# Performance work log

Measured on AMD Instinct MI355X. Metric: run time of the kernel, lower is better.

The kernel has to match this reference:

```python
import jax, jax.numpy as jnp
import numpy as np

B, T, NE = 8, 256, 64
H = 512
NH = 4
NTOKS = 32000
VOCAB = 32000


def setup_inputs() -> dict:
    key = jax.random.key(0)
    ks = jax.random.split(key, 20)
    s = 0.02
    return {
        "outp": jax.random.randint(ks[0], (B, T), 0, NTOKS),
        "ents": jax.random.normal(ks[1], (B, NE, H), jnp.float32),
        "entlens": jax.random.randint(ks[2], (B,), 1, NE),
        "emb": jax.random.normal(ks[3], (NTOKS, H), jnp.float32) * s,
        "W_ih": jax.random.normal(ks[4], (4 * H, 2 * H), jnp.float32) * s,
        "W_hh": jax.random.normal(ks[5], (4 * H, H), jnp.float32) * s,
        "b_ih": jnp.zeros((4 * H,), jnp.float32),
        "b_hh": jnp.zeros((4 * H,), jnp.float32),
        "Wq": jax.random.normal(ks[6], (H, H), jnp.float32) * s,
        "Wk": jax.random.normal(ks[7], (H, H), jnp.float32) * s,
        "Wv": jax.random.normal(ks[8], (H, H), jnp.float32) * s,
        "out_W": jax.random.normal(ks[9], (VOCAB, 2 * H), jnp.float32) * s,
        "out_b": jnp.zeros((VOCAB,), jnp.float32),
        "sw_W": jax.random.normal(ks[10], (1, 2 * H), jnp.float32) * s,
        "sw_b": jnp.zeros((1,), jnp.float32),
        "mattn_W": jax.random.normal(ks[11], (H, 2 * H), jnp.float32) * s,
        "mattn_b": jnp.zeros((H,), jnp.float32),
    }


def reference(outp, ents, entlens, emb, W_ih, W_hh, b_ih, b_hh, Wq, Wk, Wv,
              out_W, out_b, sw_W, sw_b, mattn_W, mattn_b):
    b, ne, h = ents.shape
    hd = h // NH
    # maskFromList: valid where arange(ne) <= entlens; True = masked out
    invalid = jnp.arange(ne)[None, :] > entlens[:, None]  # [B, NE]
    neg = jnp.float32(-1e30)

    hx0 = ents.mean(axis=1)  # glob init (non-graph path)
    cx0 = hx0
    # precompute K, V per head (keys = ents)
    K = (ents @ Wk.T).reshape(b, ne, NH, hd)
    V = (ents @ Wv.T).reshape(b, ne, NH, hd)
    scale = 1.0 / jnp.sqrt(jnp.float32(h))  # GraphWriter scales by sqrt(full key_dim)

    def mha(hx):
        q = (hx @ Wq.T).reshape(b, NH, hd)
        att = jnp.einsum('bhd,bnhd->bhn', q, K) * scale
        att = jnp.where(invalid[:, None, :], neg, att)
        att = jax.nn.softmax(att, axis=-1)
        return jnp.einsum('bhn,bnhd->bhd', att, V).reshape(b, h)

    e_t = jnp.swapaxes(emb[outp], 0, 1)  # [T, B, H]

    def step(carry, k):
        hx, cx, a = carry
        prev = jnp.concatenate([a, k], axis=1)  # [B, 2H]
        gates = prev @ W_ih.T + b_ih + hx @ W_hh.T + b_hh
        i, f, g, o = jnp.split(gates, 4, axis=1)
        cx = jax.nn.sigmoid(f) * cx + jax.nn.sigmoid(i) * jnp.tanh(g)
        hx = jax.nn.sigmoid(o) * jnp.tanh(cx)
        a = mha(hx)
        return (hx, cx, a), jnp.concatenate([hx, a], axis=1)

    _, outs = jax.lax.scan(step, (hx0, cx0, jnp.zeros_like(hx0)), e_t)
    l = jnp.swapaxes(outs, 0, 1)  # [B, T, 2H]

    s = jax.nn.sigmoid(l @ sw_W.T + sw_b)                     # [B, T, 1]
    o = jax.nn.softmax(l @ out_W.T + out_b, axis=2) * s       # [B, T, V]
    # MatrixAttn pointer distribution over entities
    dec = l @ mattn_W.T + mattn_b                             # [B, T, H]
    unnorm = jnp.einsum('bth,bnh->btn', dec, ents)
    unnorm = jnp.where(invalid[:, None, :], neg, unnorm)
    z = jax.nn.softmax(unnorm, axis=2) * (1.0 - s)            # [B, T, NE]
    full = jnp.concatenate([o, z], axis=2) + 1e-6
    return jnp.log(full), z
```

## Files before the change

### kernel.cpp

```cpp
#include <hip/hip_runtime.h>
#include <cstdint>

#define TT 256
#define BB 8
#define NE 64
#define HH 512
#define VOCAB 32000
#define G4 2048
#define RS 32064
#define MROWS 2048
#define SCALE 0.044194173824159216f

typedef _Float16 h2 __attribute__((ext_vector_type(2)));
typedef _Float16 h8 __attribute__((ext_vector_type(8)));
typedef float f4 __attribute__((ext_vector_type(4)));
typedef unsigned long long u64;

__device__ inline float sigf(float x){ return 1.f/(1.f+__expf(-x)); }

__device__ inline u64 g64load(const u64* p){
  return __hip_atomic_load((u64*)p, __ATOMIC_RELAXED, __HIP_MEMORY_SCOPE_AGENT);
}
__device__ inline void g64store(u64* p, u64 v){
  __hip_atomic_store(p, v, __ATOMIC_RELAXED, __HIP_MEMORY_SCOPE_AGENT);
}

__global__ __launch_bounds__(256) void cast_k(const float* __restrict__ src, _Float16* __restrict__ dst,
    int total, int src_ld, int src_off, int dst_ld, int dst_off, int cshift, int lo, float mul, int tr)
{
  int i = blockIdx.x*256 + threadIdx.x;
  if (i >= total) return;
  int c = i & ((1<<cshift)-1);
  int r = i >> cshift;
  float x = src[(long)r*src_ld + src_off + c] * mul;
  _Float16 h = (_Float16)x;
  if (lo) h = (_Float16)(x - (float)h);
  if (tr) dst[(long)c*dst_ld + dst_off + r] = h;
  else    dst[(long)r*dst_ld + dst_off + c] = h;
}

__global__ __launch_bounds__(256) void embgather_k(const float* __restrict__ emb,
    const int* __restrict__ outp, _Float16* __restrict__ dst)
{
  int i = blockIdx.x*256 + threadIdx.x;
  int k = i & 511; int m = i >> 9;
  int t = m >> 3, b = m & 7;
  int tok = outp[b*TT + t];
  dst[i] = (_Float16)emb[(long)tok*HH + k];
}

__global__ __launch_bounds__(256) void prep_k(const float* __restrict__ b_ih, const float* __restrict__ b_hh,
    const float* __restrict__ ents, float* bsum, u64* hxe, u64* Se)
{
  int i = blockIdx.x*256 + threadIdx.x;
  if (i < G4) bsum[i] = b_ih[i] + b_hh[i];
  if (i < BB*HH) {
    int b = i >> 9, j = i & 511;
    float s = 0.f;
    for (int n = 0; n < NE; n++) s += ents[(size_t)((b<<6)+n)*HH + j];
    s *= (1.0f/NE);
    hxe[i] = (u64)__float_as_uint(s);
  }
  if (i < BB*256) Se[i] = 0ull;
}

__global__ __launch_bounds__(256) void vblk_k(const float* __restrict__ Vb,
    _Float16* __restrict__ VblkS, _Float16* __restrict__ VblkT)
{
  int i = blockIdx.x*256 + threadIdx.x;
  int he = i & 255, d = (i >> 8) & 511, b = i >> 17;
  _Float16 v = (_Float16)0.f;
  if ((he >> 6) == (d >> 7)) v = (_Float16)Vb[(((long)((b<<6)|(he&63)))<<9) + d];
  VblkT[(((long)((b<<9)|d))<<8) + he] = v;
  VblkS[(((long)((b<<8)|he))<<9) + d] = v;
}

__global__ __launch_bounds__(256) void gemm_k(const _Float16* __restrict__ A, const _Float16* __restrict__ Bm,
    float* __restrict__ C, const float* __restrict__ bias,
    int M, int N, int K, int lda, int ldb, int ldc, int accum, long sA, long sB, long sC)
{
  __shared__ __align__(16) _Float16 At[128][40];
  __shared__ __align__(16) _Float16 Bt[128][40];
  int z = blockIdx.z;
  A  += (long)z * sA;  Bm += (long)z * sB;  C += (long)z * sC;
  int tid = threadIdx.x;
  int n0 = blockIdx.x * 128, m0 = blockIdx.y * 128;
  int wave = tid >> 6, lane = tid & 63;
  int mw = (wave & 1) << 6, nw = (wave >> 1) << 6;
  int lr = tid >> 2, lc = (tid & 3) << 3;
  const _Float16* Ap0 = A + (long)(m0 + lr)*lda + lc;
  const _Float16* Ap1 = Ap0 + (long)64*lda;
  const _Float16* Bp0 = Bm + (long)(n0 + lr)*ldb + lc;
  const _Float16* Bp1 = Bp0 + (long)64*ldb;
  f4 acc[4][4] = {};
  int rr = lane & 15, kq = (lane >> 4) << 3;
  for (int kt = 0; kt < K; kt += 32) {
    h8 av0 = *(const h8*)(Ap0 + kt);
    h8 av1 = *(const h8*)(Ap1 + kt);
    h8 bv0 = *(const h8*)(Bp0 + kt);
    h8 bv1 = *(const h8*)(Bp1 + kt);
    __syncthreads();
    *(h8*)&At[lr][lc]    = av0;
    *(h8*)&At[64+lr][lc] = av1;
    *(h8*)&Bt[lr][lc]    = bv0;
    *(h8*)&Bt[64+lr][lc] = bv1;
    __syncthreads();
    h8 af[4], bf[4];
    #pragma unroll
    for (int mt=0;mt<4;mt++) af[mt] = *(const h8*)&At[mw + mt*16 + rr][kq];
    #pragma unroll
    for (int nt=0;nt<4;nt++) bf[nt] = *(const h8*)&Bt[nw + nt*16 + rr][kq];
    #pragma unroll
    for (int mt=0;mt<4;mt++)
      #pragma unroll
      for (int nt=0;nt<4;nt++)
        acc[mt][nt] = __builtin_amdgcn_mfma_f32_16x16x32_f16(af[mt], bf[nt], acc[mt][nt], 0, 0, 0);
  }
  int cc = lane & 15, rq = (lane >> 4) << 2;
  #pragma unroll
  for (int nt=0;nt<4;nt++) {
    int col = n0 + nw + nt*16 + cc;
    float bv = bias ? bias[col] : 0.f;
    #pragma unroll
    for (int mt=0;mt<4;mt++) {
      int row0 = m0 + mw + mt*16 + rq;
      #pragma unroll
      for (int r=0;r<4;r++) {
        long idx = (long)(row0 + r)*ldc + col;
        float v = acc[mt][nt][r] + bv;
        if (accum) C[idx] += v; else C[idx] = v;
      }
    }
  }
}

__global__ __launch_bounds__(512, 1) void rnn_k(
    const float* __restrict__ gates_pre, const _Float16* __restrict__ Whh16,
    const float* __restrict__ Mh, const float* __restrict__ WVall,
    const int* __restrict__ entlens,
    u64* hxe, u64* Se, _Float16* Pg, _Float16* l_h, _Float16* l_lo)
{
  __shared__ __align__(16) _Float16 Wl2[32768];
  __shared__ __align__(16) _Float16 WVl2[16384];
  __shared__ __align__(16) float    Ml2[8][512];
  __shared__ __align__(16) float    hxs[512];
  __shared__ __align__(16) _Float16 hxh[512];
  __shared__ __align__(16) _Float16 ph[256];
  __shared__ float part[4][64];
  __shared__ float gsum[64];
  __shared__ float gpl[64];

  const int tid = threadIdx.x, wg = blockIdx.x;
  const int b = wg >> 5, wgl = wg & 31, u_off = wgl << 4;
  const int lane = tid & 63, wv = tid >> 6;
  const int el = entlens[b];
  const int h_own = wgl >> 3, e_base = (wgl & 7) << 3;
  u64* hxb = hxe + ((long)b << 9);
  u64* Sb  = Se  + ((long)b << 8);

  for (int i = tid; i < 4096; i += 512) {
    int r = i >> 6, k8c = i & 63;
    int c = k8c >> 3, sl = k8c & 7;
    int grow = ((r >> 4) << 9) + u_off + (r & 15);
    *(h8*)&Wl2[((((c << 6) + r) << 3) + sl) << 3] =
        *(const h8*)(Whh16 + ((long)grow << 9) + (k8c << 3));
  }
  for (int i = tid; i < 4096; i += 512) {
    int r = i >> 9, e = i & 511;
    Ml2[r][e] = Mh[((long)h_own << 18) + (((long)((b << 6) + e_base + r)) << 9) + e];
  }
  for (int i = tid; i < 16384; i += 512) {
    int r = i >> 8, cj = i & 255, c = cj >> 3, j = cj & 7;
    int grow = ((r >> 4) << 9) + u_off + (r & 15);
    WVl2[((((c << 6) + r) << 3) + j)] = (_Float16)WVall[((long)grow << 11) + (b << 8) + cj];
  }
  if (tid < 256) {
    u64 w0 = g64load(hxb + 2*tid), w1 = g64load(hxb + 2*tid + 1);
    float f0 = __uint_as_float((unsigned)w0), f1 = __uint_as_float((unsigned)w1);
    hxs[2*tid] = f0; hxs[2*tid+1] = f1;
    hxh[2*tid] = (_Float16)f0; hxh[2*tid+1] = (_Float16)f1;
  }
  __syncthreads();
  float cx = 0.f;
  if (wv == 0 && lane < 16) cx = hxs[u_off + lane];

  for (int it = 0; it < TT; it++) {
    const unsigned set = (unsigned)(it + 1);
    {
      float sp = 0.f;
      #pragma unroll
      for (int j = 0; j < 8; j++) sp += hxs[(j << 6) + lane] * Ml2[wv][(j << 6) + lane];
      #pragma unroll
      for (int off = 32; off; off >>= 1) sp += __shfl_xor(sp, off);
      if (lane == 0)
        g64store(Sb + (h_own << 6) + e_base + wv, ((u64)set << 32) | (u64)__float_as_uint(sp));
    }
    if (tid < 64) {
      int col = ((tid >> 4) << 9) + u_off + (tid & 15);
      gpl[tid] = gates_pre[((long)((it << 3) + b) << 11) + col];
    }
    {
      int sl = tid & 7;
      float s = 0.f;
      #pragma unroll
      for (int c = 0; c < 8; c++) {
        union { h8 v; h2 p[4]; } a_, w_;
        a_.v = *(const h8*)&hxh[(c << 6) + (sl << 3)];
        w_.v = *(const h8*)&Wl2[((c << 9) + tid) << 3];
        #pragma unroll
        for (int p = 0; p < 4; p++) s = __builtin_amdgcn_fdot2(a_.p[p], w_.p[p], s, false);
      }
      s += __shfl_xor(s, 1); s += __shfl_xor(s, 2); s += __shfl_xor(s, 4);
      if (sl == 0) gsum[tid >> 3] = s;
    }
    if (wv < 4) {
      u64 sv = g64load(Sb + (wv << 6) + lane);
      while ((unsigned)(sv >> 32) < set) { __builtin_amdgcn_s_sleep(1); sv = g64load(Sb + (wv << 6) + lane); }
      if (it > 0) {
        float x = __uint_as_float((unsigned)sv);
        if (lane > el) x = -1e30f;
        float mx = x;
        #pragma unroll
        for (int off = 32; off; off >>= 1) mx = fmaxf(mx, __shfl_xor(mx, off));
        float e = __expf(x - mx), sm = e;
        #pragma unroll
        for (int off = 32; off; off >>= 1) sm += __shfl_xor(sm, off);
        float p = e / sm;
        _Float16 p16 = (_Float16)p;
        ph[(wv << 6) + lane] = p16;
        float s = 0.f;
        #pragma unroll
        for (int cc = 0; cc < 8; cc++) {
          int c = (wv << 3) + cc;
          union { h8 v; h2 p[4]; } pv, wv_;
          pv.v  = *(const h8*)&ph[(wv << 6) + (cc << 3)];
          wv_.v = *(const h8*)&WVl2[(((c << 6) + lane) << 3)];
          #pragma unroll
          for (int p2 = 0; p2 < 4; p2++) s = __builtin_amdgcn_fdot2(pv.p[p2], wv_.p[p2], s, false);
        }
        part[wv][lane] = s;
        Pg[((long)((b << 8) + (it - 1)) << 8) + (wv << 6) + lane] = p16;
      }
    }
    __syncthreads();
    if (wv == 0) {
      float wvp = (it > 0) ? (part[0][lane] + part[1][lane] + part[2][lane] + part[3][lane]) : 0.f;
      float gv = gpl[lane] + gsum[lane] + wvp;
      float gi = __shfl(gv, lane & 15);
      float gf = __shfl(gv, 16 + (lane & 15));
      float gg = __shfl(gv, 32 + (lane & 15));
      float go = __shfl(gv, 48 + (lane & 15));
      if (lane < 16) {
        float c_ = sigf(gf)*cx + sigf(gi)*tanhf(gg);
        cx = c_;
        float h = sigf(go)*tanhf(c_);
        int j = u_off + lane;
        g64store(hxb + j, ((u64)set << 32) | (u64)__float_as_uint(h));
        _Float16 hh_ = (_Float16)h;
        long li = ((long)((b << 8) + it)) << 10;
        l_h[li + j]  = hh_;
        l_lo[li + j] = (_Float16)(h - (float)hh_);
      }
    }
    if (tid < 256) {
      u64 w0 = g64load(hxb + 2*tid), w1 = g64load(hxb + 2*tid + 1);
      while ((unsigned)(w0 >> 32) < set) { __builtin_amdgcn_s_sleep(1); w0 = g64load(hxb + 2*tid); }
      while ((unsigned)(w1 >> 32) < set) { __builtin_amdgcn_s_sleep(1); w1 = g64load(hxb + 2*tid + 1); }
      float f0 = __uint_as_float((unsigned)w0), f1 = __uint_as_float((unsigned)w1);
      hxs[2*tid] = f0; hxs[2*tid+1] = f1;
      hxh[2*tid] = (_Float16)f0; hxh[2*tid+1] = (_Float16)f1;
    }
    __syncthreads();
  }
  {
    float sp = 0.f;
    #pragma unroll
    for (int j = 0; j < 8; j++) sp += hxs[(j << 6) + lane] * Ml2[wv][(j << 6) + lane];
    #pragma unroll
    for (int off = 32; off; off >>= 1) sp += __shfl_xor(sp, off);
    if (lane == 0)
      g64store(Sb + (h_own << 6) + e_base + wv, ((u64)257u << 32) | (u64)__float_as_uint(sp));
    if (wv < 4) {
      u64 sv = g64load(Sb + (wv << 6) + lane);
      while ((unsigned)(sv >> 32) < 257u) { __builtin_amdgcn_s_sleep(1); sv = g64load(Sb + (wv << 6) + lane); }
      float x = __uint_as_float((unsigned)sv);
      if (lane > el) x = -1e30f;
      float mx = x;
      #pragma unroll
      for (int off = 32; off; off >>= 1) mx = fmaxf(mx, __shfl_xor(mx, off));
      float e = __expf(x - mx), sm = e;
      #pragma unroll
      for (int off = 32; off; off >>= 1) sm += __shfl_xor(sm, off);
      Pg[((long)((b << 8) + 255) << 8) + (wv << 6) + lane] = (_Float16)(e / sm);
    }
  }
}

__global__ __launch_bounds__(256) void stats_k(const float* __restrict__ out0,
    const _Float16* __restrict__ l_h, const float* __restrict__ swW, const float* __restrict__ swb,
    float* rowmax, float* rowsum, float* sgate)
{
  int m = blockIdx.x, tid = threadIdx.x;
  const float* row = out0 + (long)m*RS;
  float mx = -1e30f, sm = 0.f;
  for (int c = tid; c < VOCAB; c += 256) {
    float x = row[c];
    float nm = fmaxf(mx, x);
    sm = sm*__expf(mx-nm) + __expf(x-nm);
    mx = nm;
  }
  float sd = 0.f;
  const _Float16* lr_ = l_h + ((long)m << 10);
  for (int k = tid; k < 1024; k += 256) sd += (float)lr_[k] * swW[k];
  #pragma unroll
  for (int off=32; off>0; off>>=1) {
    float omx = __shfl_xor(mx, off), osm = __shfl_xor(sm, off);
    float nm = fmaxf(mx, omx);
    sm = sm*__expf(mx-nm) + osm*__expf(omx-nm);
    mx = nm;
    sd += __shfl_xor(sd, off);
  }
  __shared__ float smx[4], ssm[4], ssd[4];
  int wv = tid >> 6;
  if ((tid & 63) == 0) { smx[wv]=mx; ssm[wv]=sm; ssd[wv]=sd; }
  __syncthreads();
  if (tid == 0) {
    float M = smx[0], S = ssm[0], D = ssd[0];
    for (int w2=1;w2<4;w2++) {
      float nm = fmaxf(M, smx[w2]);
      S = S*__expf(M-nm) + ssm[w2]*__expf(smx[w2]-nm);
      M = nm; D += ssd[w2];
    }
    rowmax[m] = M; rowsum[m] = S;
    sgate[m] = 1.f/(1.f + __expf(-(D + swb[0])));
  }
}

__global__ __launch_bounds__(256) void fin_k(float* __restrict__ out,
    const float* __restrict__ dec, const float* __restrict__ ents, const int* __restrict__ entlens,
    const float* __restrict__ rowmax, const float* __restrict__ rowsum, const float* __restrict__ sgate)
{
  int m = blockIdx.x, tid = threadIdx.x;
  int b = m >> 8;
  __shared__ float dl[512];
  for (int i = tid; i < 512; i += 256) dl[i] = dec[((long)m<<9) + i];
  __syncthreads();
  float s = sgate[m];
  if (tid < 64) {
    int n = tid;
    const float* ep = ents + (((long)((b<<6)+n)) << 9);
    float uq = 0.f;
    for (int k=0;k<512;k+=4)
      uq += dl[k]*ep[k] + dl[k+1]*ep[k+1] + dl[k+2]*ep[k+2] + dl[k+3]*ep[k+3];
    if (n > entlens[b]) uq = -1e30f;
    float mx = uq;
    #pragma unroll
    for (int off=32; off>0; off>>=1) mx = fmaxf(mx, __shfl_xor(mx, off));
    float e = __expf(uq - mx);
    float sum = e;
    #pragma unroll
    for (int off=32; off>0; off>>=1) sum += __shfl_xor(sum, off);
    float z = (e/sum) * (1.f - s);
    out[(long)m*RS + VOCAB + n] = __logf(z + 1e-6f);
    out[(long)MROWS*RS + ((long)m<<6) + n] = z;
  }
  float mx = rowmax[m], inv = 1.f/rowsum[m];
  for (int c = tid; c < VOCAB; c += 256) {
    long idx = (long)m*RS + c;
    float x = out[idx];
    out[idx] = __logf(__expf(x - mx)*inv*s + 1e-6f);
  }
}

extern "C" void kernel_launch(void* const* d_in, const int* in_sizes, int n_in,
                              void* d_out, int out_size, void* d_ws, size_t ws_size,
                              hipStream_t stream)
{
  const int*   outp    = (const int*)d_in[0];
  const float* ents    = (const float*)d_in[1];
  const int*   entlens = (const int*)d_in[2];
  const float* emb     = (const float*)d_in[3];
  const float* W_ih    = (const float*)d_in[4];
  const float* W_hh    = (const float*)d_in[5];
  const float* b_ih    = (const float*)d_in[6];
  const float* b_hh    = (const float*)d_in[7];
  const float* Wq      = (const float*)d_in[8];
  const float* Wk      = (const float*)d_in[9];
  const float* Wv      = (const float*)d_in[10];
  const float* out_W   = (const float*)d_in[11];
  const float* out_b   = (const float*)d_in[12];
  const float* sw_W    = (const float*)d_in[13];
  const float* sw_b    = (const float*)d_in[14];
  const float* mattn_W = (const float*)d_in[15];
  const float* mattn_b = (const float*)d_in[16];
  float* out = (float*)d_out;
  (void)in_sizes; (void)n_in; (void)out_size; (void)ws_size;

  char* w = (char*)d_ws;
  size_t off = 0;
  auto alloc = [&](size_t bytes) -> char* {
    char* p = w + off; off += bytes; off = (off + 255) & ~(size_t)255; return p;
  };
  _Float16* outW_h = (_Float16*)alloc((size_t)VOCAB*1024*2);
  _Float16* l_h    = (_Float16*)alloc((size_t)MROWS*1024*2);
  _Float16* l_lo   = (_Float16*)alloc((size_t)MROWS*1024*2);
  float*    gpre   = (float*)alloc((size_t)MROWS*2048*4);
  _Float16* Wihk_h = (_Float16*)alloc((size_t)2048*512*2);
  _Float16* Wiha16 = (_Float16*)alloc((size_t)2048*512*2);
  _Float16* Whh16  = (_Float16*)alloc((size_t)2048*512*2);
  _Float16* emb_h  = (_Float16*)alloc((size_t)2048*512*2);
  _Float16* ents_h = (_Float16*)alloc((size_t)512*512*2);
  _Float16* Wk_h   = (_Float16*)alloc((size_t)512*512*2);
  _Float16* Wv_h   = (_Float16*)alloc((size_t)512*512*2);
  _Float16* WqT16  = (_Float16*)alloc((size_t)512*512*2);
  _Float16* mat_h  = (_Float16*)alloc((size_t)512*1024*2);
  _Float16* mat_lo = (_Float16*)alloc((size_t)512*1024*2);
  float*    Kb     = (float*)alloc((size_t)512*512*4);
  float*    Vb     = (float*)alloc((size_t)512*512*4);
  _Float16* Kb16   = (_Float16*)alloc((size_t)512*512*2);
  float*    Mh     = (float*)alloc((size_t)4*512*512*4);
  _Float16* VblkS  = (_Float16*)alloc((size_t)2048*512*2);
  _Float16* VblkT  = (_Float16*)alloc((size_t)8*512*256*2);
  float*    WVall  = (float*)alloc((size_t)2048*2048*4);
  _Float16* Pg     = (_Float16*)alloc((size_t)8*256*256*2);
  float*    dec    = (float*)alloc((size_t)MROWS*512*4);
  float*    bsum   = (float*)alloc(2048*4);
  u64*      hxe    = (u64*)alloc((size_t)4096*8);
  u64*      Se     = (u64*)alloc((size_t)2048*8);
  float*    rmax   = (float*)alloc(2048*4);
  float*    rsum   = (float*)alloc(2048*4);
  float*    sg     = (float*)alloc(2048*4);
  float*    Af     = gpre;

  auto cast = [&](const float* s, _Float16* d, int total, int sld, int soff, int dld, int doff,
                  int cs, int lo, float mul, int tr) {
    cast_k<<<(total+255)/256, 256, 0, stream>>>(s, d, total, sld, soff, dld, doff, cs, lo, mul, tr);
  };
  auto gemm = [&](const _Float16* A, const _Float16* B, float* C, const float* bias,
                  int M, int N, int K, int lda, int ldb, int ldc, int accum,
                  int gx, int gy, int gz, long sA, long sB, long sC) {
    gemm_k<<<dim3(gx,gy,gz), 256, 0, stream>>>(A, B, C, bias, M, N, K, lda, ldb, ldc, accum, sA, sB, sC);
  };

  cast(out_W,   outW_h, VOCAB*1024, 1024, 0,   1024, 0,   10, 0, 1.f, 0);
  cast(W_ih,    Wihk_h, 2048*512,   1024, 512, 512,  0,   9,  0, 1.f, 0);
  cast(W_ih,    Wiha16, 2048*512,   1024, 0,   512,  0,   9,  0, 1.f, 0);
  cast(W_hh,    Whh16,  2048*512,   512,  0,   512,  0,   9,  0, 1.f, 0);
  cast(Wq,      WqT16,  512*512,    512,  0,   512,  0,   9,  0, 1.f, 1);
  cast(Wk,      Wk_h,   512*512,    512,  0,   512,  0,   9,  0, 1.f, 0);
  cast(Wv,      Wv_h,   512*512,    512,  0,   512,  0,   9,  0, 1.f, 0);
  cast(mattn_W, mat_h,  512*1024,   1024, 0,   1024, 0,   10, 0, 1.f, 0);
  cast(mattn_W, mat_lo, 512*1024,   1024, 0,   1024, 0,   10, 1, 1.f, 0);
  cast(ents,    ents_h, 512*512,    512,  0,   512,  0,   9,  0, 1.f, 0);

  embgather_k<<<4096, 256, 0, stream>>>(emb, outp, emb_h);
  prep_k<<<16, 256, 0, stream>>>(b_ih, b_hh, ents, bsum, hxe, Se);

  gemm(ents_h, Wk_h,   Kb,   nullptr, 512,  512,  512, 512, 512, 512,  0,  4,  4, 1, 0,0,0);
  gemm(ents_h, Wv_h,   Vb,   nullptr, 512,  512,  512, 512, 512, 512,  0,  4,  4, 1, 0,0,0);
  gemm(emb_h,  Wihk_h, gpre, bsum,    2048, 2048, 512, 512, 512, 2048, 0, 16, 16, 1, 0,0,0);

  cast(Kb, Kb16, 512*512, 512, 0, 512, 0, 9, 0, SCALE, 0);
  vblk_k<<<4096, 256, 0, stream>>>(Vb, VblkS, VblkT);

  for (int h = 0; h < 4; h++)
    gemm(Kb16 + h*128, WqT16 + h*128, Mh + (long)h*512*512, nullptr,
         512, 512, 128, 512, 512, 512, 0, 4, 4, 1, 0,0,0);
  gemm(Wiha16, VblkS, WVall, nullptr,
       2048, 2048, 512, 512, 512, 2048, 0, 16, 16, 1, 0,0,0);

  rnn_k<<<256, 512, 0, stream>>>(gpre, Whh16, Mh, WVall, entlens, hxe, Se, Pg, l_h, l_lo);

  gemm(Pg, VblkT, Af, nullptr, 256, 512, 256, 256, 256, 512, 0,
       4, 2, 8, (long)256*256, (long)512*256, (long)256*512);
  cast(Af, l_h,  MROWS*512, 512, 0, 1024, 512, 9, 0, 1.f, 0);
  cast(Af, l_lo, MROWS*512, 512, 0, 1024, 512, 9, 1, 1.f, 0);

  gemm(l_h,  mat_h,  dec, mattn_b, 2048, 512,   1024, 1024, 1024, 512, 0, 4,  16, 1, 0,0,0);
  gemm(l_lo, mat_h,  dec, nullptr, 2048, 512,   1024, 1024, 1024, 512, 1, 4,  16, 1, 0,0,0);
  gemm(l_h,  mat_lo, dec, nullptr, 2048, 512,   1024, 1024, 1024, 512, 1, 4,  16, 1, 0,0,0);
  gemm(l_h,  outW_h, out, out_b,   2048, 32000, 1024, 1024, 1024, RS,  0, 250, 16, 1, 0,0,0);

  stats_k<<<2048, 256, 0, stream>>>(out, l_h, sw_W, sw_b, rmax, rsum, sg);
  fin_k<<<2048, 256, 0, stream>>>(out, dec, ents, entlens, rmax, rsum, sg);
}
```

Baseline: 2.032 ms.

## Batch casts, load GEMM tiles directly to LDS, fuse stats/finalize kernels

Merges the ten weight-cast launches into one descriptor-driven kernel. Batches the K/V projection GEMMs and the four per-head Mh GEMMs through the z grid dimension. Switches the GEMM tile staging to global_load_lds direct-to-LDS copies in an unpadded layout. Fuses the softmax stats and finalize kernels into one kernel that caches each 32000-wide logit row in LDS, cutting a full read of the large output buffer and several launches. The unpadded LDS layout may add bank conflicts, the ~128KB LDS per block limits occupancy, and the batched K/V GEMM assumes Wk_h/Wv_h and Kb/Vb are laid out contiguously.

```diff
diff --git a/kernel.cpp b/kernel.cpp
--- a/kernel.cpp
+++ b/kernel.cpp
@@ -25,6 +25,32 @@
   __hip_atomic_store(p, v, __ATOMIC_RELAXED, __HIP_MEMORY_SCOPE_AGENT);
 }
 
+__device__ __forceinline__ void cp16(const _Float16* g, _Float16* l) {
+  __builtin_amdgcn_global_load_lds(
+      (__attribute__((address_space(1))) void*)(g),
+      (__attribute__((address_space(3))) void*)(l), 16, 0, 0);
+}
+
+struct CDesc { const float* src; _Float16* dst; int total, sld, soff, dld, doff, cs, lo, tr; float mul; };
+struct CPack { CDesc d[10]; int boff[11]; };
+
+__global__ __launch_bounds__(256) void castall_k(CPack p)
+{
+  int blk = blockIdx.x;
+  int di = 0;
+  while (blk >= p.boff[di+1]) di++;
+  CDesc d = p.d[di];
+  int i = (blk - p.boff[di])*256 + threadIdx.x;
+  if (i >= d.total) return;
+  int c = i & ((1<<d.cs)-1);
+  int r = i >> d.cs;
+  float x = d.src[(long)r*d.sld + d.soff + c] * d.mul;
+  _Float16 h = (_Float16)x;
+  if (d.lo) h = (_Float16)(x - (float)h);
+  if (d.tr) d.dst[(long)c*d.dld + d.doff + r] = h;
+  else      d.dst[(long)r*d.dld + d.doff + c] = h;
+}
+
 __global__ __launch_bounds__(256) void cast_k(const float* __restrict__ src, _Float16* __restrict__ dst,
     int total, int src_ld, int src_off, int dst_ld, int dst_off, int cshift, int lo, float mul, int tr)
 {
@@ -79,37 +105,36 @@
     float* __restrict__ C, const float* __restrict__ bias,
     int M, int N, int K, int lda, int ldb, int ldc, int accum, long sA, long sB, long sC)
 {
-  __shared__ __align__(16) _Float16 At[128][40];
-  __shared__ __align__(16) _Float16 Bt[128][40];
+  __shared__ __align__(16) _Float16 At[128*32];
+  __shared__ __align__(16) _Float16 Bt[128*32];
   int z = blockIdx.z;
   A  += (long)z * sA;  Bm += (long)z * sB;  C += (long)z * sC;
   int tid = threadIdx.x;
   int n0 = blockIdx.x * 128, m0 = blockIdx.y * 128;
   int wave = tid >> 6, lane = tid & 63;
   int mw = (wave & 1) << 6, nw = (wave >> 1) << 6;
-  int lr = tid >> 2, lc = (tid & 3) << 3;
-  const _Float16* Ap0 = A + (long)(m0 + lr)*lda + lc;
-  const _Float16* Ap1 = Ap0 + (long)64*lda;
-  const _Float16* Bp0 = Bm + (long)(n0 + lr)*ldb + lc;
-  const _Float16* Bp1 = Bp0 + (long)64*ldb;
+  int srow = (wave << 5) + (lane >> 2);
+  int scol = (lane & 3) << 3;
+  const _Float16* Ag0 = A + (long)(m0 + srow)*lda + scol;
+  const _Float16* Ag1 = Ag0 + (long)16*lda;
+  const _Float16* Bg0 = Bm + (long)(n0 + srow)*ldb + scol;
+  const _Float16* Bg1 = Bg0 + (long)16*ldb;
+  _Float16* Ald = At + (wave << 10);
+  _Float16* Bld = Bt + (wave << 10);
   f4 acc[4][4] = {};
   int rr = lane & 15, kq = (lane >> 4) << 3;
   for (int kt = 0; kt < K; kt += 32) {
-    h8 av0 = *(const h8*)(Ap0 + kt);
-    h8 av1 = *(const h8*)(Ap1 + kt);
-    h8 bv0 = *(const h8*)(Bp0 + kt);
-    h8 bv1 = *(const h8*)(Bp1 + kt);
     __syncthreads();
-    *(h8*)&At[lr][lc]    = av0;
-    *(h8*)&At[64+lr][lc] = av1;
-    *(h8*)&Bt[lr][lc]    = bv0;
-    *(h8*)&Bt[64+lr][lc] = bv1;
+    cp16(Ag0 + kt, Ald);
+    cp16(Ag1 + kt, Ald + 512);
+    cp16(Bg0 + kt, Bld);
+    cp16(Bg1 + kt, Bld + 512);
     __syncthreads();
     h8 af[4], bf[4];
     #pragma unroll
-    for (int mt=0;mt<4;mt++) af[mt] = *(const h8*)&At[mw + mt*16 + rr][kq];
-    #pragma unroll
-    for (int nt=0;nt<4;nt++) bf[nt] = *(const h8*)&Bt[nw + nt*16 + rr][kq];
+    for (int mt=0;mt<4;mt++) af[mt] = *(const h8*)&At[((mw + mt*16 + rr) << 5) + kq];
+    #pragma unroll
+    for (int nt=0;nt<4;nt++) bf[nt] = *(const h8*)&Bt[((nw + nt*16 + rr) << 5) + kq];
     #pragma unroll
     for (int mt=0;mt<4;mt++)
       #pragma unroll
@@ -296,79 +321,77 @@
   }
 }
 
-__global__ __launch_bounds__(256) void stats_k(const float* __restrict__ out0,
+__global__ __launch_bounds__(256) void statsfin_k(float* __restrict__ out,
     const _Float16* __restrict__ l_h, const float* __restrict__ swW, const float* __restrict__ swb,
-    float* rowmax, float* rowsum, float* sgate)
-{
+    const float* __restrict__ dec, const float* __restrict__ ents, const int* __restrict__ entlens)
+{
+  __shared__ __align__(16) float rowb[VOCAB];
+  __shared__ float dl[512];
+  __shared__ float red[3][4];
+  __shared__ float bc[3];
   int m = blockIdx.x, tid = threadIdx.x;
-  const float* row = out0 + (long)m*RS;
-  float mx = -1e30f, sm = 0.f;
-  for (int c = tid; c < VOCAB; c += 256) {
-    float x = row[c];
-    float nm = fmaxf(mx, x);
-    sm = sm*__expf(mx-nm) + __expf(x-nm);
-    mx = nm;
-  }
+  int b = m >> 8;
+  float* row = out + (long)m*RS;
+  float mx = -1e30f;
+  for (int c4 = tid; c4 < 8000; c4 += 256) {
+    f4 v = *(const f4*)(row + ((long)c4 << 2));
+    *(f4*)&rowb[c4 << 2] = v;
+    mx = fmaxf(mx, fmaxf(fmaxf(v[0], v[1]), fmaxf(v[2], v[3])));
+  }
+  for (int i = tid; i < 512; i += 256) dl[i] = dec[((long)m << 9) + i];
   float sd = 0.f;
   const _Float16* lr_ = l_h + ((long)m << 10);
   for (int k = tid; k < 1024; k += 256) sd += (float)lr_[k] * swW[k];
+  int wv = tid >> 6;
   #pragma unroll
-  for (int off=32; off>0; off>>=1) {
-    float omx = __shfl_xor(mx, off), osm = __shfl_xor(sm, off);
-    float nm = fmaxf(mx, omx);
-    sm = sm*__expf(mx-nm) + osm*__expf(omx-nm);
-    mx = nm;
-    sd += __shfl_xor(sd, off);
-  }
-  __shared__ float smx[4], ssm[4], ssd[4];
-  int wv = tid >> 6;
-  if ((tid & 63) == 0) { smx[wv]=mx; ssm[wv]=sm; ssd[wv]=sd; }
+  for (int off = 32; off; off >>= 1) { mx = fmaxf(mx, __shfl_xor(mx, off)); sd += __shfl_xor(sd, off); }
+  if ((tid & 63) == 0) { red[0][wv] = mx; red[1][wv] = sd; }
   __syncthreads();
   if (tid == 0) {
-    float M = smx[0], S = ssm[0], D = ssd[0];
-    for (int w2=1;w2<4;w2++) {
-      float nm = fmaxf(M, smx[w2]);
-      S = S*__expf(M-nm) + ssm[w2]*__expf(smx[w2]-nm);
-      M = nm; D += ssd[w2];
-    }
-    rowmax[m] = M; rowsum[m] = S;
-    sgate[m] = 1.f/(1.f + __expf(-(D + swb[0])));
-  }
-}
-
-__global__ __launch_bounds__(256) void fin_k(float* __restrict__ out,
-    const float* __restrict__ dec, const float* __restrict__ ents, const int* __restrict__ entlens,
-    const float* __restrict__ rowmax, const float* __restrict__ rowsum, const float* __restrict__ sgate)
-{
-  int m = blockIdx.x, tid = threadIdx.x;
-  int b = m >> 8;
-  __shared__ float dl[512];
-  for (int i = tid; i < 512; i += 256) dl[i] = dec[((long)m<<9) + i];
+    bc[0] = fmaxf(fmaxf(red[0][0], red[0][1]), fmaxf(red[0][2], red[0][3]));
+    float D_ = red[1][0] + red[1][1] + red[1][2] + red[1][3];
+    bc[2] = 1.f/(1.f + __expf(-(D_ + swb[0])));
+  }
   __syncthreads();
-  float s = sgate[m];
+  float MX = bc[0];
+  float sm = 0.f;
+  for (int c4 = tid; c4 < 8000; c4 += 256) {
+    f4 v = *(const f4*)&rowb[c4 << 2];
+    #pragma unroll
+    for (int j = 0; j < 4; j++) v[j] = __expf(v[j] - MX);
+    sm += v[0] + v[1] + v[2] + v[3];
+    *(f4*)&rowb[c4 << 2] = v;
+  }
+  #pragma unroll
+  for (int off = 32; off; off >>= 1) sm += __shfl_xor(sm, off);
+  if ((tid & 63) == 0) red[2][wv] = sm;
+  __syncthreads();
+  if (tid == 0) bc[1] = 1.f/(red[2][0] + red[2][1] + red[2][2] + red[2][3]);
+  __syncthreads();
+  float s = bc[2], inv = bc[1];
   if (tid < 64) {
     int n = tid;
-    const float* ep = ents + (((long)((b<<6)+n)) << 9);
+    const float* ep = ents + (((long)((b << 6) + n)) << 9);
     float uq = 0.f;
-    for (int k=0;k<512;k+=4)
+    for (int k = 0; k < 512; k += 4)
       uq += dl[k]*ep[k] + dl[k+1]*ep[k+1] + dl[k+2]*ep[k+2] + dl[k+3]*ep[k+3];
     if (n > entlens[b]) uq = -1e30f;
-    float mx = uq;
-    #pragma unroll
-    for (int off=32; off>0; off>>=1) mx = fmaxf(mx, __shfl_xor(mx, off));
-    float e = __expf(uq - mx);
+    float mxz = uq;
+    #pragma unroll
+    for (int off = 32; off; off >>= 1) mxz = fmaxf(mxz, __shfl_xor(mxz, off));
+    float e = __expf(uq - mxz);
     float sum = e;
     #pragma unroll
-    for (int off=32; off>0; off>>=1) sum += __shfl_xor(sum, off);
+    for (int off = 32; off; off >>= 1) sum += __shfl_xor(sum, off);
     float z = (e/sum) * (1.f - s);
     out[(long)m*RS + VOCAB + n] = __logf(z + 1e-6f);
-    out[(long)MROWS*RS + ((long)m<<6) + n] = z;
-  }
-  float mx = rowmax[m], inv = 1.f/rowsum[m];
-  for (int c = tid; c < VOCAB; c += 256) {
-    long idx = (long)m*RS + c;
-    float x = out[idx];
-    out[idx] = __logf(__expf(x - mx)*inv*s + 1e-6f);
+    out[(long)MROWS*RS + ((long)m << 6) + n] = z;
+  }
+  for (int c4 = tid; c4 < 8000; c4 += 256) {
+    f4 v = *(const f4*)&rowb[c4 << 2];
+    #pragma unroll
+    for (int j = 0; j < 4; j++) v[j] = __logf(v[j]*inv*s + 1e-6f);
+    *(f4*)(row + ((long)c4 << 2)) = v;
   }
 }
 
@@ -427,45 +450,49 @@
   float*    bsum   = (float*)alloc(2048*4);
   u64*      hxe    = (u64*)alloc((size_t)4096*8);
   u64*      Se     = (u64*)alloc((size_t)2048*8);
-  float*    rmax   = (float*)alloc(2048*4);
-  float*    rsum   = (float*)alloc(2048*4);
-  float*    sg     = (float*)alloc(2048*4);
   float*    Af     = gpre;
 
-  auto cast = [&](const float* s, _Float16* d, int total, int sld, int soff, int dld, int doff,
-                  int cs, int lo, float mul, int tr) {
-    cast_k<<<(total+255)/256, 256, 0, stream>>>(s, d, total, sld, soff, dld, doff, cs, lo, mul, tr);
-  };
   auto gemm = [&](const _Float16* A, const _Float16* B, float* C, const float* bias,
                   int M, int N, int K, int lda, int ldb, int ldc, int accum,
                   int gx, int gy, int gz, long sA, long sB, long sC) {
     gemm_k<<<dim3(gx,gy,gz), 256, 0, stream>>>(A, B, C, bias, M, N, K, lda, ldb, ldc, accum, sA, sB, sC);
   };
-
-  cast(out_W,   outW_h, VOCAB*1024, 1024, 0,   1024, 0,   10, 0, 1.f, 0);
-  cast(W_ih,    Wihk_h, 2048*512,   1024, 512, 512,  0,   9,  0, 1.f, 0);
-  cast(W_ih,    Wiha16, 2048*512,   1024, 0,   512,  0,   9,  0, 1.f, 0);
-  cast(W_hh,    Whh16,  2048*512,   512,  0,   512,  0,   9,  0, 1.f, 0);
-  cast(Wq,      WqT16,  512*512,    512,  0,   512,  0,   9,  0, 1.f, 1);
-  cast(Wk,      Wk_h,   512*512,    512,  0,   512,  0,   9,  0, 1.f, 0);
-  cast(Wv,      Wv_h,   512*512,    512,  0,   512,  0,   9,  0, 1.f, 0);
-  cast(mattn_W, mat_h,  512*1024,   1024, 0,   1024, 0,   10, 0, 1.f, 0);
-  cast(mattn_W, mat_lo, 512*1024,   1024, 0,   1024, 0,   10, 1, 1.f, 0);
-  cast(ents,    ents_h, 512*512,    512,  0,   512,  0,   9,  0, 1.f, 0);
+  auto cast = [&](const float* s, _Float16* d, int total, int sld, int soff, int dld, int doff,
+                  int cs, int lo, float mul, int tr) {
+    cast_k<<<(total+255)/256, 256, 0, stream>>>(s, d, total, sld, soff, dld, doff, cs, lo, mul, tr);
+  };
+
+  CPack cp;
+  auto setd = [&](int i, const float* s, _Float16* d, int total, int sld, int soff, int dld, int doff,
+                  int cs, int lo, int tr, float mul) {
+    cp.d[i] = CDesc{ s, d, total, sld, soff, dld, doff, cs, lo, tr, mul };
+  };
+  setd(0, out_W,   outW_h, VOCAB*1024, 1024, 0,   1024, 0,   10, 0, 0, 1.f);
+  setd(1, W_ih,    Wihk_h, 2048*512,   1024, 512, 512,  0,   9,  0, 0, 1.f);
+  setd(2, W_ih,    Wiha16, 2048*512,   1024, 0,   512,  0,   9,  0, 0, 1.f);
+  setd(3, W_hh,    Whh16,  2048*512,   512,  0,   512,  0,   9,  0, 0, 1.f);
+  setd(4, Wq,      WqT16,  512*512,    512,  0,   512,  0,   9,  0, 1, 1.f);
+  setd(5, Wk,      Wk_h,   512*512,    512,  0,   512,  0,   9,  0, 0, 1.f);
+  setd(6, Wv,      Wv_h,   512*512,    512,  0,   512,  0,   9,  0, 0, 1.f);
+  setd(7, mattn_W, mat_h,  512*1024,   1024, 0,   1024, 0,   10, 0, 0, 1.f);
+  setd(8, mattn_W, mat_lo, 512*1024,   1024, 0,   1024, 0,   10, 1, 0, 1.f);
+  setd(9, ents,    ents_h, 512*512,    512,  0,   512,  0,   9,  0, 0, 1.f);
+  cp.boff[0] = 0;
+  for (int i = 0; i < 10; i++) cp.boff[i+1] = cp.boff[i] + (cp.d[i].total + 255)/256;
+  castall_k<<<cp.boff[10], 256, 0, stream>>>(cp);
 
   embgather_k<<<4096, 256, 0, stream>>>(emb, outp, emb_h);
   prep_k<<<16, 256, 0, stream>>>(b_ih, b_hh, ents, bsum, hxe, Se);
 
-  gemm(ents_h, Wk_h,   Kb,   nullptr, 512,  512,  512, 512, 512, 512,  0,  4,  4, 1, 0,0,0);
-  gemm(ents_h, Wv_h,   Vb,   nullptr, 512,  512,  512, 512, 512, 512,  0,  4,  4, 1, 0,0,0);
-  gemm(emb_h,  Wihk_h, gpre, bsum,    2048, 2048, 512, 512, 512, 2048, 0, 16, 16, 1, 0,0,0);
+  gemm(ents_h, Wk_h, Kb, nullptr, 512, 512, 512, 512, 512, 512, 0,
+       4, 4, 2, 0, (long)512*512, (long)512*512);
+  gemm(emb_h, Wihk_h, gpre, bsum, 2048, 2048, 512, 512, 512, 2048, 0, 16, 16, 1, 0,0,0);
 
   cast(Kb, Kb16, 512*512, 512, 0, 512, 0, 9, 0, SCALE, 0);
   vblk_k<<<4096, 256, 0, stream>>>(Vb, VblkS, VblkT);
 
-  for (int h = 0; h < 4; h++)
-    gemm(Kb16 + h*128, WqT16 + h*128, Mh + (long)h*512*512, nullptr,
-         512, 512, 128, 512, 512, 512, 0, 4, 4, 1, 0,0,0);
+  gemm(Kb16, WqT16, Mh, nullptr, 512, 512, 128, 512, 512, 512, 0,
+       4, 4, 4, 128, 128, (long)512*512);
   gemm(Wiha16, VblkS, WVall, nullptr,
        2048, 2048, 512, 512, 512, 2048, 0, 16, 16, 1, 0,0,0);
 
@@ -481,6 +508,5 @@
   gemm(l_h,  mat_lo, dec, nullptr, 2048, 512,   1024, 1024, 1024, 512, 1, 4,  16, 1, 0,0,0);
   gemm(l_h,  outW_h, out, out_b,   2048, 32000, 1024, 1024, 1024, RS,  0, 250, 16, 1, 0,0,0);
 
-  stats_k<<<2048, 256, 0, stream>>>(out, l_h, sw_W, sw_b, rmax, rsum, sg);
-  fin_k<<<2048, 256, 0, stream>>>(out, dec, ents, entlens, rmax, rsum, sg);
-}
+  statsfin_k<<<2048, 256, 0, stream>>>(out, l_h, sw_W, sw_b, dec, ents, entlens);
+}
```

New measurement: 2.090 ms. +2.9%, slower.
